# Optimization experiments

Hardware: AMD Instinct MI355X
Metric: run time of the kernel (lower is better)

Reference implementation:

```python
import jax, jax.numpy as jnp
import numpy as np

B, L = 4096, 64          # batch, patch_len
OUT, KS, K = 64, 8, 4    # out_planes, kernel_size, num mixtures
STRIDE = 1
TEMP = 34.0
L_OUT = (L - KS) // STRIDE + 1   # 57
C = OUT * L_OUT                  # BN feature dim = 3648
HIDDEN = int(L * 0.5) + 1        # attention hidden planes = 33
EPS = 1e-5


def _gelu(x):
    return jax.nn.gelu(x, approximate=False)  # torch nn.GELU default = exact erf


def setup_inputs() -> dict:
    key = jax.random.key(0)
    ks = jax.random.split(key, 8)
    return {
        "x": jax.random.normal(ks[0], (B, L), jnp.float32),
        "fc1_w": jax.random.normal(ks[1], (HIDDEN, L), jnp.float32) * (2.0 / HIDDEN) ** 0.5,
        "fc2_w": jax.random.normal(ks[2], (K, HIDDEN), jnp.float32) * (2.0 / K) ** 0.5,
        "fc2_b": jnp.zeros((K,), jnp.float32),
        "weight": jax.random.normal(ks[3], (K, OUT, KS), jnp.float32) * 0.1,
        "bias": jnp.zeros((K, OUT), jnp.float32),
        "bn_gamma": jnp.ones((C,), jnp.float32),
        "bn_beta": jnp.zeros((C,), jnp.float32),
    }


def reference(x, fc1_w, fc2_w, fc2_b, weight, bias, bn_gamma, bn_beta):
    # --- attention1d: 1x1 convs over the patch_len 'channel' dim == linears ---
    a = _gelu(x @ fc1_w.T)                 # [B, HIDDEN]
    logits = a @ fc2_w.T + fc2_b           # [B, K]
    attn = jax.nn.softmax(logits / TEMP, axis=1)

    # --- sliding windows (im2col), shared by both conv paths ---
    idx = jnp.arange(L_OUT)[:, None] * STRIDE + jnp.arange(KS)[None, :]
    frames = x[:, idx]                     # [B, L_OUT, KS]

    # --- kernel_wise: full conv with each of the K kernels ---
    kw = jnp.einsum('blc,koc->bolk', frames, weight) + bias.T[None, :, None, :]  # [B,OUT,L_OUT,K]
    kw = kw.reshape(B, C, K)

    # --- per-sample aggregated kernel + grouped (per-sample) conv ---
    agg_w = jnp.einsum('bk,koc->boc', attn, weight)      # [B, OUT, KS]
    agg_b = attn @ bias                                  # [B, OUT]
    out = jnp.einsum('blc,boc->bol', frames, agg_w) + agg_b[:, :, None]  # [B,OUT,L_OUT]
    out = out.reshape(B, C)

    # --- BN(GELU(.)) with batch statistics (training-mode BatchNorm1d) ---
    g = _gelu(out)
    m = g.mean(axis=0)
    v = g.var(axis=0)
    out = (g - m) * jax.lax.rsqrt(v + EPS) * bn_gamma + bn_beta

    g2 = _gelu(kw)                                        # [B, C, K]
    m2 = g2.mean(axis=(0, 2), keepdims=True)
    v2 = g2.var(axis=(0, 2), keepdims=True)
    kw = (g2 - m2) * jax.lax.rsqrt(v2 + EPS) * bn_gamma[None, :, None] + bn_beta[None, :, None]

    return out, attn, kw.transpose(0, 2, 1)              # [B,C], [B,K], [B,K,C]
```

## Files before the change

### kernel.cpp

```cpp
#include <hip/hip_runtime.h>
#include <cstddef>

#define B_     4096
#define L_     64
#define OUT_   64
#define KS_    8
#define KK_    4
#define LOUT_  57
#define C_     3648
#define HID_   33
#define TEMP_  34.0f
#define EPS_   1e-5f
#define NCH_   128
#define SROWS_ 32
#define NB2_   32

__device__ __forceinline__ float gelu_f(float x) {
    float e = exp2f(-2.3022083f * x * fmaf(0.044715f * x, x, 1.0f));
    return x * __builtin_amdgcn_rcpf(1.0f + e);
}

template<int ROWS>
__device__ __forceinline__ void stage_shifted(
    const float* __restrict__ x, int b0, int tid,
    float4 (*xs4)[ROWS][17])
{
    for (int idx = tid; idx < ROWS * 16; idx += 256) {
        int r = idx >> 4, t = idx & 15;
        const float4* xrow = (const float4*)(x + (size_t)(b0 + r) * L_);
        float4 a  = xrow[t];
        float4 bq = xrow[t < 15 ? t + 1 : 15];
        xs4[0][r][t] = a;
        xs4[1][r][t] = make_float4(a.y, a.z, a.w, bq.x);
        xs4[2][r][t] = make_float4(a.z, a.w, bq.x, bq.y);
        xs4[3][r][t] = make_float4(a.w, bq.x, bq.y, bq.z);
    }
}

__global__ __launch_bounds__(128) void attn_kernel(
    const float* __restrict__ x, const float* __restrict__ fc1_w,
    const float* __restrict__ fc2_w, const float* __restrict__ fc2_b,
    float* __restrict__ attn_out)
{
    __shared__ float fc1s[HID_][L_];
    __shared__ float fc2s[KK_][HID_];
    __shared__ float fc2bs[KK_];
    int tid = threadIdx.x;
    for (int i = tid; i < HID_ * L_; i += 128) fc1s[i / L_][i % L_] = fc1_w[i];
    for (int i = tid; i < KK_ * HID_; i += 128) fc2s[i / HID_][i % HID_] = fc2_w[i];
    if (tid < KK_) fc2bs[tid] = fc2_b[tid];
    __syncthreads();

    int b = blockIdx.x * 128 + tid;
    if (b >= B_) return;

    float xr[L_];
    const float4* xp = (const float4*)(x + (size_t)b * L_);
    #pragma unroll
    for (int i = 0; i < L_ / 4; ++i) {
        float4 v = xp[i];
        xr[4*i] = v.x; xr[4*i+1] = v.y; xr[4*i+2] = v.z; xr[4*i+3] = v.w;
    }
    float logit[KK_] = {0.f, 0.f, 0.f, 0.f};
    for (int h = 0; h < HID_; ++h) {
        const float4* fr = (const float4*)&fc1s[h][0];
        float acc = 0.f;
        #pragma unroll
        for (int i = 0; i < L_ / 4; ++i) {
            float4 wv = fr[i];
            acc = fmaf(xr[4*i],   wv.x, acc);
            acc = fmaf(xr[4*i+1], wv.y, acc);
            acc = fmaf(xr[4*i+2], wv.z, acc);
            acc = fmaf(xr[4*i+3], wv.w, acc);
        }
        float a = gelu_f(acc);
        #pragma unroll
        for (int k = 0; k < KK_; ++k) logit[k] = fmaf(a, fc2s[k][h], logit[k]);
    }
    float z[KK_];
    #pragma unroll
    for (int k = 0; k < KK_; ++k) z[k] = (logit[k] + fc2bs[k]) * (1.0f / TEMP_);
    float mx = fmaxf(fmaxf(z[0], z[1]), fmaxf(z[2], z[3]));
    float e[KK_]; float s = 0.f;
    #pragma unroll
    for (int k = 0; k < KK_; ++k) { e[k] = __expf(z[k] - mx); s += e[k]; }
    float inv = __builtin_amdgcn_rcpf(s);
    #pragma unroll
    for (int k = 0; k < KK_; ++k) attn_out[(size_t)b * KK_ + k] = e[k] * inv;
}

__global__ __launch_bounds__(256) void stats_kernel(
    const float* __restrict__ x, const float* __restrict__ weight,
    const float* __restrict__ bias, const float* __restrict__ attn,
    float* __restrict__ P, int use_partial)
{
    int cb = blockIdx.x;
    int chunk = blockIdx.y;
    int tid = threadIdx.x;
    int c = cb * 256 + tid;
    bool act = c < C_;
    int o = act ? (c / LOUT_) : 0;
    int l = act ? (c - o * LOUT_) : 0;
    int q = l >> 2, s = l & 3;

    float w[KK_][KS_];
    float bk[KK_];
    #pragma unroll
    for (int k = 0; k < KK_; ++k) {
        bk[k] = bias[k * OUT_ + o];
        #pragma unroll
        for (int cq = 0; cq < KS_; ++cq) w[k][cq] = weight[(k * OUT_ + o) * KS_ + cq];
    }

    __shared__ float4 xs4[4][SROWS_][17];
    __shared__ float at[SROWS_][KK_];

    int b0 = chunk * SROWS_;
    stage_shifted<SROWS_>(x, b0, tid, xs4);
    if (tid < SROWS_ * KK_) ((float*)at)[tid] = attn[(size_t)b0 * KK_ + tid];
    __syncthreads();

    float s1 = 0.f, s2 = 0.f, t1 = 0.f, t2 = 0.f;
    if (act) {
        const float4* base = &xs4[s][0][q];
        #pragma unroll 4
        for (int r = 0; r < SROWS_; ++r) {
            float4 A  = base[(size_t)r * 17];
            float4 Bv = base[(size_t)r * 17 + 1];
            float xw[8] = {A.x, A.y, A.z, A.w, Bv.x, Bv.y, Bv.z, Bv.w};
            float kv0 = bk[0], kv1 = bk[1], kv2 = bk[2], kv3 = bk[3];
            #pragma unroll
            for (int cq = 0; cq < KS_; ++cq) {
                float xv = xw[cq];
                kv0 = fmaf(xv, w[0][cq], kv0);
                kv1 = fmaf(xv, w[1][cq], kv1);
                kv2 = fmaf(xv, w[2][cq], kv2);
                kv3 = fmaf(xv, w[3][cq], kv3);
            }
            float ov = at[r][0] * kv0;
            ov = fmaf(at[r][1], kv1, ov);
            ov = fmaf(at[r][2], kv2, ov);
            ov = fmaf(at[r][3], kv3, ov);
            float g = gelu_f(ov);
            s1 += g; s2 = fmaf(g, g, s2);
            float g0 = gelu_f(kv0), g1 = gelu_f(kv1), g2 = gelu_f(kv2), g3 = gelu_f(kv3);
            t1 += g0 + g1 + g2 + g3;
            t2 = fmaf(g0, g0, t2); t2 = fmaf(g1, g1, t2);
            t2 = fmaf(g2, g2, t2); t2 = fmaf(g3, g3, t2);
        }
    }
    if (!act) return;
    if (use_partial) {
        size_t base = (size_t)chunk * 4 * C_ + c;
        P[base]          = s1;
        P[base + C_]     = s2;
        P[base + 2 * C_] = t1;
        P[base + 3 * C_] = t2;
    } else {
        atomicAdd(&P[c], s1);
        atomicAdd(&P[C_ + c], s2);
        atomicAdd(&P[2 * C_ + c], t1);
        atomicAdd(&P[3 * C_ + c], t2);
    }
}

__global__ __launch_bounds__(256) void finalize_kernel(
    const float* __restrict__ P, const float* __restrict__ gamma,
    const float* __restrict__ beta, float* __restrict__ F, int use_partial)
{
    __shared__ float red[4][64];
    int t = threadIdx.x;
    int cl = t & 63;
    int s = t >> 6;
    int c = blockIdx.x * 64 + cl;
    float a = 0.f;
    if (use_partial) {
        for (int ch = 0; ch < NCH_; ++ch)
            a += P[((size_t)ch * 4 + s) * C_ + c];
    } else {
        a = P[(size_t)s * C_ + c];
    }
    red[s][cl] = a;
    __syncthreads();
    if (t < 64) {
        float a0 = red[0][cl], a1 = red[1][cl], a2 = red[2][cl], a3 = red[3][cl];
        float m  = a0 * (1.0f / B_);
        float v  = a1 * (1.0f / B_) - m * m;
        float rs = rsqrtf(v + EPS_);
        float m2 = a2 * (1.0f / (B_ * KK_));
        float v2 = a3 * (1.0f / (B_ * KK_)) - m2 * m2;
        float rs2 = rsqrtf(v2 + EPS_);
        float ga = gamma[c], be = beta[c];
        F[c]          = rs * ga;
        F[C_ + c]     = be - m * rs * ga;
        F[2 * C_ + c] = rs2 * ga;
        F[3 * C_ + c] = be - m2 * rs2 * ga;
    }
}

__global__ __launch_bounds__(256) void write_kernel(
    const float* __restrict__ x, const float* __restrict__ weight,
    const float* __restrict__ bias, const float* __restrict__ attn,
    const float* __restrict__ F,
    float* __restrict__ out0, float* __restrict__ kwout)
{
    int cc = blockIdx.x;
    int bg = blockIdx.y;
    int tid = threadIdx.x;
    int c = cc * 256 + tid;
    bool act = c < C_;
    int o = act ? (c / LOUT_) : 0;
    int l = act ? (c - o * LOUT_) : 0;
    int q = l >> 2, s = l & 3;

    float w[KK_][KS_];
    float bk[KK_];
    #pragma unroll
    for (int k = 0; k < KK_; ++k) {
        bk[k] = bias[k * OUT_ + o];
        #pragma unroll
        for (int cq = 0; cq < KS_; ++cq) w[k][cq] = weight[(k * OUT_ + o) * KS_ + cq];
    }
    float sA = 0.f, hA = 0.f, sK = 0.f, hK = 0.f;
    if (act) {
        sA = F[c]; hA = F[C_ + c]; sK = F[2 * C_ + c]; hK = F[3 * C_ + c];
    }

    __shared__ float4 xs4[4][NB2_][17];
    __shared__ float at[NB2_][KK_];
    int b0 = bg * NB2_;
    stage_shifted<NB2_>(x, b0, tid, xs4);
    if (tid < NB2_ * KK_) ((float*)at)[tid] = attn[(size_t)b0 * KK_ + tid];
    __syncthreads();

    if (!act) return;

    const float4* xbase = &xs4[s][0][q];
    #pragma unroll 4
    for (int r = 0; r < NB2_; ++r) {
        float4 A  = xbase[(size_t)r * 17];
        float4 Bv = xbase[(size_t)r * 17 + 1];
        float xw[8] = {A.x, A.y, A.z, A.w, Bv.x, Bv.y, Bv.z, Bv.w};
        float kv0 = bk[0], kv1 = bk[1], kv2 = bk[2], kv3 = bk[3];
        #pragma unroll
        for (int cq = 0; cq < KS_; ++cq) {
            float xv = xw[cq];
            kv0 = fmaf(xv, w[0][cq], kv0);
            kv1 = fmaf(xv, w[1][cq], kv1);
            kv2 = fmaf(xv, w[2][cq], kv2);
            kv3 = fmaf(xv, w[3][cq], kv3);
        }
        float ov = at[r][0] * kv0;
        ov = fmaf(at[r][1], kv1, ov);
        ov = fmaf(at[r][2], kv2, ov);
        ov = fmaf(at[r][3], kv3, ov);
        int b = b0 + r;
        float g = gelu_f(ov);
        out0[(size_t)b * C_ + c] = fmaf(g, sA, hA);
        float g0 = gelu_f(kv0), g1 = gelu_f(kv1), g2v = gelu_f(kv2), g3 = gelu_f(kv3);
        float* base = kwout + (size_t)b * KK_ * C_ + c;
        base[0]      = fmaf(g0,  sK, hK);
        base[C_]     = fmaf(g1,  sK, hK);
        base[2 * C_] = fmaf(g2v, sK, hK);
        base[3 * C_] = fmaf(g3,  sK, hK);
    }
}

extern "C" void kernel_launch(void* const* d_in, const int* in_sizes, int n_in,
                              void* d_out, int out_size, void* d_ws, size_t ws_size,
                              hipStream_t stream) {
    const float* x      = (const float*)d_in[0];
    const float* fc1_w  = (const float*)d_in[1];
    const float* fc2_w  = (const float*)d_in[2];
    const float* fc2_b  = (const float*)d_in[3];
    const float* weight = (const float*)d_in[4];
    const float* bias   = (const float*)d_in[5];
    const float* gamma  = (const float*)d_in[6];
    const float* beta   = (const float*)d_in[7];

    float* out  = (float*)d_out;
    float* out0 = out;
    float* attn = out + (size_t)B_ * C_;
    float* kwout = attn + (size_t)B_ * KK_;

    size_t need = (size_t)(NCH_ * 4 + 4) * C_ * sizeof(float);
    int use_partial = ws_size >= need;
    float* P = (float*)d_ws;
    float* F = P + (use_partial ? (size_t)NCH_ * 4 * C_ : (size_t)4 * C_);
    if (!use_partial)
        hipMemsetAsync(P, 0, 4 * C_ * sizeof(float), stream);

    attn_kernel<<<B_ / 128, 128, 0, stream>>>(x, fc1_w, fc2_w, fc2_b, attn);
    stats_kernel<<<dim3((C_ + 255) / 256, NCH_), 256, 0, stream>>>(
        x, weight, bias, attn, P, use_partial);
    finalize_kernel<<<C_ / 64, 256, 0, stream>>>(P, gamma, beta, F, use_partial);
    write_kernel<<<dim3((C_ + 255) / 256, B_ / NB2_), 256, 0, stream>>>(
        x, weight, bias, attn, F, out0, kwout);
}
```

Measured before the change: 145.7 us.

## Fuse attention MLP and softmax into the stats kernel to drop a launch

Removes the separate attention kernel and computes the attention MLP, GELU and softmax inside each stats_kernel block. It works on the 32 rows already staged in shared memory, with 8 lanes per row splitting the hidden units and combining by shuffle. Only blocks with cb==0 write attn to global memory for the later write kernel. This saves a launch and a dependency, but repeats the attention computation in every column block (15x redundant) and reads fc1_w straight from global memory rather than from shared memory.

```diff
diff --git a/kernel.cpp b/kernel.cpp
--- a/kernel.cpp
+++ b/kernel.cpp
@@ -37,62 +37,11 @@
     }
 }
 
-__global__ __launch_bounds__(128) void attn_kernel(
+__global__ __launch_bounds__(256) void stats_kernel(
     const float* __restrict__ x, const float* __restrict__ fc1_w,
     const float* __restrict__ fc2_w, const float* __restrict__ fc2_b,
-    float* __restrict__ attn_out)
-{
-    __shared__ float fc1s[HID_][L_];
-    __shared__ float fc2s[KK_][HID_];
-    __shared__ float fc2bs[KK_];
-    int tid = threadIdx.x;
-    for (int i = tid; i < HID_ * L_; i += 128) fc1s[i / L_][i % L_] = fc1_w[i];
-    for (int i = tid; i < KK_ * HID_; i += 128) fc2s[i / HID_][i % HID_] = fc2_w[i];
-    if (tid < KK_) fc2bs[tid] = fc2_b[tid];
-    __syncthreads();
-
-    int b = blockIdx.x * 128 + tid;
-    if (b >= B_) return;
-
-    float xr[L_];
-    const float4* xp = (const float4*)(x + (size_t)b * L_);
-    #pragma unroll
-    for (int i = 0; i < L_ / 4; ++i) {
-        float4 v = xp[i];
-        xr[4*i] = v.x; xr[4*i+1] = v.y; xr[4*i+2] = v.z; xr[4*i+3] = v.w;
-    }
-    float logit[KK_] = {0.f, 0.f, 0.f, 0.f};
-    for (int h = 0; h < HID_; ++h) {
-        const float4* fr = (const float4*)&fc1s[h][0];
-        float acc = 0.f;
-        #pragma unroll
-        for (int i = 0; i < L_ / 4; ++i) {
-            float4 wv = fr[i];
-            acc = fmaf(xr[4*i],   wv.x, acc);
-            acc = fmaf(xr[4*i+1], wv.y, acc);
-            acc = fmaf(xr[4*i+2], wv.z, acc);
-            acc = fmaf(xr[4*i+3], wv.w, acc);
-        }
-        float a = gelu_f(acc);
-        #pragma unroll
-        for (int k = 0; k < KK_; ++k) logit[k] = fmaf(a, fc2s[k][h], logit[k]);
-    }
-    float z[KK_];
-    #pragma unroll
-    for (int k = 0; k < KK_; ++k) z[k] = (logit[k] + fc2bs[k]) * (1.0f / TEMP_);
-    float mx = fmaxf(fmaxf(z[0], z[1]), fmaxf(z[2], z[3]));
-    float e[KK_]; float s = 0.f;
-    #pragma unroll
-    for (int k = 0; k < KK_; ++k) { e[k] = __expf(z[k] - mx); s += e[k]; }
-    float inv = __builtin_amdgcn_rcpf(s);
-    #pragma unroll
-    for (int k = 0; k < KK_; ++k) attn_out[(size_t)b * KK_ + k] = e[k] * inv;
-}
-
-__global__ __launch_bounds__(256) void stats_kernel(
-    const float* __restrict__ x, const float* __restrict__ weight,
-    const float* __restrict__ bias, const float* __restrict__ attn,
-    float* __restrict__ P, int use_partial)
+    const float* __restrict__ weight, const float* __restrict__ bias,
+    float* __restrict__ attn_out, float* __restrict__ P, int use_partial)
 {
     int cb = blockIdx.x;
     int chunk = blockIdx.y;
@@ -117,7 +66,54 @@
 
     int b0 = chunk * SROWS_;
     stage_shifted<SROWS_>(x, b0, tid, xs4);
-    if (tid < SROWS_ * KK_) ((float*)at)[tid] = attn[(size_t)b0 * KK_ + tid];
+    __syncthreads();
+
+    {
+        int r = tid >> 3, j = tid & 7;
+        float lg0 = 0.f, lg1 = 0.f, lg2 = 0.f, lg3 = 0.f;
+        const float4* xr4 = &xs4[0][r][0];
+        for (int h = j; h < HID_; h += 8) {
+            const float4* f4 = (const float4*)(fc1_w + (size_t)h * L_);
+            float acc = 0.f;
+            #pragma unroll
+            for (int i = 0; i < L_ / 4; ++i) {
+                float4 xv = xr4[i];
+                float4 wv = f4[i];
+                acc = fmaf(xv.x, wv.x, acc);
+                acc = fmaf(xv.y, wv.y, acc);
+                acc = fmaf(xv.z, wv.z, acc);
+                acc = fmaf(xv.w, wv.w, acc);
+            }
+            float a = gelu_f(acc);
+            lg0 = fmaf(a, fc2_w[0 * HID_ + h], lg0);
+            lg1 = fmaf(a, fc2_w[1 * HID_ + h], lg1);
+            lg2 = fmaf(a, fc2_w[2 * HID_ + h], lg2);
+            lg3 = fmaf(a, fc2_w[3 * HID_ + h], lg3);
+        }
+        #pragma unroll
+        for (int mask = 1; mask < 8; mask <<= 1) {
+            lg0 += __shfl_xor(lg0, mask, 8);
+            lg1 += __shfl_xor(lg1, mask, 8);
+            lg2 += __shfl_xor(lg2, mask, 8);
+            lg3 += __shfl_xor(lg3, mask, 8);
+        }
+        if (j == 0) {
+            float z0 = (lg0 + fc2_b[0]) * (1.0f / TEMP_);
+            float z1 = (lg1 + fc2_b[1]) * (1.0f / TEMP_);
+            float z2 = (lg2 + fc2_b[2]) * (1.0f / TEMP_);
+            float z3 = (lg3 + fc2_b[3]) * (1.0f / TEMP_);
+            float mx = fmaxf(fmaxf(z0, z1), fmaxf(z2, z3));
+            float e0 = __expf(z0 - mx), e1 = __expf(z1 - mx);
+            float e2 = __expf(z2 - mx), e3 = __expf(z3 - mx);
+            float inv = __builtin_amdgcn_rcpf(e0 + e1 + e2 + e3);
+            float a0 = e0 * inv, a1 = e1 * inv, a2 = e2 * inv, a3 = e3 * inv;
+            at[r][0] = a0; at[r][1] = a1; at[r][2] = a2; at[r][3] = a3;
+            if (cb == 0) {
+                float4* ap = (float4*)(attn_out + (size_t)(b0 + r) * KK_);
+                *ap = make_float4(a0, a1, a2, a3);
+            }
+        }
+    }
     __syncthreads();
 
     float s1 = 0.f, s2 = 0.f, t1 = 0.f, t2 = 0.f;
@@ -290,9 +286,8 @@
     if (!use_partial)
         hipMemsetAsync(P, 0, 4 * C_ * sizeof(float), stream);
 
-    attn_kernel<<<B_ / 128, 128, 0, stream>>>(x, fc1_w, fc2_w, fc2_b, attn);
     stats_kernel<<<dim3((C_ + 255) / 256, NCH_), 256, 0, stream>>>(
-        x, weight, bias, attn, P, use_partial);
+        x, fc1_w, fc2_w, fc2_b, weight, bias, attn, P, use_partial);
     finalize_kernel<<<C_ / 64, 256, 0, stream>>>(P, gamma, beta, F, use_partial);
     write_kernel<<<dim3((C_ + 255) / 256, B_ / NB2_), 256, 0, stream>>>(
         x, weight, bias, attn, F, out0, kwout);
```

Measured after the change: 166.3 us. 1.14x slower.
